# Performance work log

Measured on AMD Instinct MI355X. Metric: run time of the kernel, lower is better.

Reference implementation:

```python
import jax, jax.numpy as jnp
import numpy as np

EPS = 1e-5

def _ln(x, g, b):
    mu = jnp.mean(x, axis=-1, keepdims=True)
    var = jnp.mean((x - mu) ** 2, axis=-1, keepdims=True)
    return (x - mu) / jnp.sqrt(var + EPS) * g + b

def _aft(x, q_w, q_b, k_w, k_b, v_w, v_b, p_w, p_b, wbias):
    # AFTFull: Yt = sigmoid(Q) * (exp(wbias) @ (exp(K)*V)) / (exp(wbias) @ exp(K))
    T = x.shape[1]
    Q = x @ q_w + q_b
    K = x @ k_w + k_b
    V = x @ v_w + v_b
    ew = jnp.exp(wbias[:T, :T])                      # [T, T]
    eK = jnp.exp(K)                                   # [B, T, H]
    num = jnp.einsum('ts,bsh->bth', ew, eK * V)
    den = jnp.einsum('ts,bsh->bth', ew, eK)
    Yt = jax.nn.sigmoid(Q) * (num / den)
    return Yt @ p_w + p_b

def setup_inputs() -> dict:
    key = jax.random.key(0)
    B, T, D, H = 8, 2048, 256, 256
    MAXT = 2048
    std = 1.0 / np.sqrt(H)
    names_shapes = [
        ('fc_w', (D, H)), ('fc_b', (H,)),
        ('q_w', (H, H)), ('q_b', (H,)),
        ('k_w', (H, H)), ('k_b', (H,)),
        ('v_w', (H, H)), ('v_b', (H,)),
        ('p_w', (H, H)), ('p_b', (H,)),
        ('wbias', (MAXT, MAXT)),
        ('n1_g', (H,)), ('n1_b', (H,)),
        ('n2_g', (H,)), ('n2_b', (H,)),
        ('w_i', (H, H)), ('u_i', (H, H)), ('b_i', (H,)),
        ('w_f', (H, H)), ('u_f', (H, H)), ('b_f', (H,)),
        ('w_c', (H, H)), ('u_c', (H, H)), ('b_c', (H,)),
        ('w_o', (H, H)), ('u_o', (H, H)), ('b_o', (H,)),
    ]
    keys = jax.random.split(key, len(names_shapes) + 1)
    inp = {'x': jax.random.normal(keys[0], (B, T, D), dtype=jnp.float32)}
    for k, (name, shp) in zip(keys[1:], names_shapes):
        inp[name] = jax.random.uniform(k, shp, dtype=jnp.float32, minval=-std, maxval=std)
    return inp

def reference(x, fc_w, fc_b, q_w, q_b, k_w, k_b, v_w, v_b, p_w, p_b, wbias,
              n1_g, n1_b, n2_g, n2_b,
              w_i, u_i, b_i, w_f, u_f, b_f, w_c, u_c, b_c, w_o, u_o, b_o):
    xf = x @ fc_w + fc_b                              # [B, T, H]
    att = _aft(xf, q_w, q_b, k_w, k_b, v_w, v_b, p_w, p_b, wbias)
    # original calls self.norm(x_) but discards the result -> only relu applies
    filt = jax.nn.relu(att)
    afx = _ln(att, n1_g, n1_b)
    prod = _ln(filt * afx, n2_g, n2_b)                # [B, T, H]
    B, T, H = prod.shape
    h0 = jnp.zeros((B, H), prod.dtype)
    c0 = jnp.zeros((B, H), prod.dtype)
    def step(carry, x_t):
        h, c = carry
        i = jax.nn.sigmoid(x_t @ w_i + h @ u_i + b_i)
        f = jax.nn.sigmoid(x_t @ w_f + h @ u_f + b_f)
        g = jnp.tanh(x_t @ w_c + h @ u_c + b_c)
        o = jax.nn.sigmoid(x_t @ w_o + h @ u_o + b_o)
        c = f * c + i * g
        h = o * jnp.tanh(c)
        return (h, c), h
    (h_t, c_t), hs = jax.lax.scan(step, (h0, c0), prod.transpose(1, 0, 2))
    hidden_seq = hs.transpose(1, 0, 2)                # [B, T, H]
    return hidden_seq, h_t, c_t
```

## Files before the change

### kernel.cpp

```cpp
#include <hip/hip_runtime.h>


typedef unsigned short u16;
typedef unsigned int   u32;
typedef u16 u16x4 __attribute__((ext_vector_type(4)));
typedef u16 u16x8 __attribute__((ext_vector_type(8)));
typedef u32 u32x2 __attribute__((ext_vector_type(2)));
typedef u32 u32x4 __attribute__((ext_vector_type(4)));
typedef short s16x8 __attribute__((ext_vector_type(8)));
typedef float f32x4 __attribute__((ext_vector_type(4)));
typedef _Float16 f16x2 __attribute__((ext_vector_type(2)));

typedef __attribute__((address_space(3))) void* lds_vp;
typedef const __attribute__((address_space(1))) void* gbl_vp;
#define GLDS(gp, lp) __builtin_amdgcn_global_load_lds((gbl_vp)(gp), (lds_vp)(lp), 16, 0, 0)

__device__ __forceinline__ float b2f(u16 u){
  union { u32 i; float f; } c; c.i = ((u32)u) << 16; return c.f;
}
__device__ __forceinline__ u16 f2b(float f){
  union { float f; u32 i; } c; c.f = f;
  u32 i = c.i;
  return (u16)((i + 0x7FFFu + ((i >> 16) & 1u)) >> 16);
}
__device__ __forceinline__ u16 f2h_bits(float f){
  _Float16 h = (_Float16)f;
  return __builtin_bit_cast(u16, h);
}
__device__ __forceinline__ float dot2(u32 a, u32 b, float acc){
#if __has_builtin(__builtin_amdgcn_fdot2)
  return __builtin_amdgcn_fdot2(__builtin_bit_cast(f16x2, a),
                                __builtin_bit_cast(f16x2, b), acc, false);
#else
  f16x2 x = __builtin_bit_cast(f16x2, a), y = __builtin_bit_cast(f16x2, b);
  return acc + (float)x[0]*(float)y[0] + (float)x[1]*(float)y[1];
#endif
}
__device__ __forceinline__ float sigm(float x){ return 1.f/(1.f + __expf(-x)); }
__device__ __forceinline__ float tanh_f(float x){
  float e = __expf(-2.f * fmaxf(x, -44.f));
  return (1.f - e)/(1.f + e);
}

__global__ void k_detect(const u16* __restrict__ x, int* __restrict__ flag){
  const int l = threadIdx.x;
  const u16 u = x[l];
  const float v = b2f(u);
  const int bad = !(v == v) || fabsf(v) > 1e4f || (v != 0.f && fabsf(v) < 1e-30f);
  const int zev = ((l & 1) == 0) && (u == 0);
  unsigned long long mb = __ballot(bad);
  unsigned long long mz = __ballot(zev);
  if (l == 0) *flag = (mb != 0ull || __popcll(mz) >= 24) ? 1 : 0;
}

__global__ __launch_bounds__(256) void k_cvt_x(const void* __restrict__ xin,
    u16* __restrict__ xb, const int* __restrict__ flag){
  const int isf = *flag;
  const size_t e = ((size_t)blockIdx.x*256 + threadIdx.x)*8;
  u16x8 o;
  if (isf){
    const float* p = (const float*)xin + e;
    f32x4 a = *(const f32x4*)p, b = *(const f32x4*)(p+4);
    o[0]=f2b(a[0]);o[1]=f2b(a[1]);o[2]=f2b(a[2]);o[3]=f2b(a[3]);
    o[4]=f2b(b[0]);o[5]=f2b(b[1]);o[6]=f2b(b[2]);o[7]=f2b(b[3]);
  } else {
    o = *(const u16x8*)((const u16*)xin + e);
  }
  *(u16x8*)(xb + e) = o;
}

template<int EPI>
__global__ __launch_bounds__(256)
void k_gemm(const u16* __restrict__ A, const u16* __restrict__ Bt,
            void* __restrict__ C, const u16* __restrict__ bias,
            const u16* __restrict__ aux,
            int M, int N, int K, int lda, int ldb, int ldc,
            long bsB , long bsC )
{
  __shared__ __align__(16) u16 As[128*32];
  __shared__ __align__(16) u16 Bs[128*32];
  const int tid = threadIdx.x;
  const int wv = tid >> 6, l = tid & 63;
  const int m0 = blockIdx.x * 128, n0 = blockIdx.y * 128;
  const u16* Bp = Bt + (size_t)blockIdx.z * bsB;
  char* Cp = (char*)C + (size_t)blockIdx.z * bsC;

  const int rL = wv*16 + (l >> 2);
  const int cL = (l & 3) * 8;
  const u16* gA = A  + (size_t)(m0 + rL)*lda + cL;
  const u16* gB = Bp + (size_t)(n0 + rL)*ldb + cL;
  u16* lA = As + wv*512 + l*8;
  u16* lB = Bs + wv*512 + l*8;

  f32x4 acc[4][4];
  #pragma unroll
  for (int m=0;m<4;++m)
    #pragma unroll
    for (int n=0;n<4;++n) acc[m][n] = f32x4{0.f,0.f,0.f,0.f};

  const int wr = wv >> 1, wc = wv & 1;
  const int lr = l & 15, lk = (l >> 4) * 8, lq = l >> 4;
  const int nk = K >> 5;
  for (int kt = 0; kt < nk; ++kt){
    __syncthreads();
    GLDS(gA,                  lA);
    GLDS(gA + (size_t)64*lda, lA + 2048);
    GLDS(gB,                  lB);
    GLDS(gB + (size_t)64*ldb, lB + 2048);
    gA += 32; gB += 32;
    __syncthreads();
    s16x8 af[4], bfr[4];
    #pragma unroll
    for (int m=0;m<4;++m) af[m]  = *(const s16x8*)&As[(wr*64 + m*16 + lr)*32 + lk];
    #pragma unroll
    for (int n=0;n<4;++n) bfr[n] = *(const s16x8*)&Bs[(wc*64 + n*16 + lr)*32 + lk];
    #pragma unroll
    for (int m=0;m<4;++m)
      #pragma unroll
      for (int n=0;n<4;++n)
        acc[m][n] = __builtin_amdgcn_mfma_f32_16x16x32_bf16(af[m], bfr[n], acc[m][n], 0, 0, 0);
  }

  #pragma unroll
  for (int m=0;m<4;++m){
    const int gr0 = m0 + wr*64 + m*16 + lq*4;
    #pragma unroll
    for (int n=0;n<4;++n){
      const int gc = n0 + wc*64 + n*16 + lr;
      f32x4 v = acc[m][n];
      if constexpr (EPI == 0 || EPI == 1 || EPI == 4){
        const float bb = b2f(bias[gc]);
        u16* Cb = (u16*)Cp;
        const int cc = (EPI == 4) ? (((gc & 255) << 2) + (gc >> 8)) : gc;
        #pragma unroll
        for (int r=0;r<4;++r){
          float xv = v[r] + bb;
          if constexpr (EPI == 1) xv = sigm(xv);
          Cb[(size_t)(gr0 + r)*ldc + cc] = f2b(xv);
        }
      } else if constexpr (EPI == 2){
        u16* Cb = (u16*)Cp;
        #pragma unroll
        for (int r=0;r<4;++r) Cb[(size_t)(gr0 + r)*ldc + gc] = f2b(v[r]);
      } else {
        const float bb = b2f(bias[gc]);
        u16x4 ekv, ek;
        #pragma unroll
        for (int r=0;r<4;++r){
          float e  = __expf(v[r] + bb);
          float vv = b2f(aux[(size_t)(gr0 + r)*256 + gc]);
          ek[r]  = f2b(e);
          ekv[r] = f2b(e * vv);
        }
        const int z = gr0 >> 11, t0 = gr0 & 2047;
        u16* base = (u16*)Cp + ((size_t)z*512 + gc)*2048 + t0;
        *(u16x4*)base = ekv;
        *(u16x4*)(base + (size_t)256*2048) = ek;
      }
    }
  }
}

struct TJobs { const void* src[13]; u16* dst[13]; int mode[13]; };

__global__ __launch_bounds__(256) void k_transpose(TJobs jb, const int* __restrict__ flag){
  const int isf = *flag;
  const int mz = blockIdx.y;
  const void* in = jb.src[mz]; u16* out = jb.dst[mz]; const int mode = jb.mode[mz];
  const int bi = blockIdx.x >> 2, bj = blockIdx.x & 3;
  __shared__ float tile[64][65];
  const int tid = threadIdx.x;
  const int r = tid >> 3, c = (tid & 7) * 8;
  #pragma unroll
  for (int it=0; it<2; ++it){
    const size_t base = (size_t)(bi*64 + it*32 + r)*256 + bj*64 + c;
    float vals[8];
    if (isf){
      const float* p = (const float*)in + base;
      f32x4 a = *(const f32x4*)p, b = *(const f32x4*)(p+4);
      vals[0]=a[0];vals[1]=a[1];vals[2]=a[2];vals[3]=a[3];
      vals[4]=b[0];vals[5]=b[1];vals[6]=b[2];vals[7]=b[3];
    } else {
      u16x8 v = *(const u16x8*)((const u16*)in + base);
      #pragma unroll
      for (int u=0;u<8;++u) vals[u] = b2f(v[u]);
    }
    #pragma unroll
    for (int u=0;u<8;++u) tile[it*32 + r][c+u] = vals[u];
  }
  __syncthreads();
  #pragma unroll
  for (int it=0; it<2; ++it){
    const int rr = it*32 + r;
    u16x8 o;
    #pragma unroll
    for (int u=0;u<8;++u){
      float xv = tile[c+u][rr];
      o[u] = mode ? f2h_bits(xv) : f2b(xv);
    }
    *(u16x8*)(out + (size_t)(bj*64 + rr)*256 + bi*64 + c) = o;
  }
}

struct PJobs { const void* src[13]; };

__global__ __launch_bounds__(256) void k_pack_params(PJobs pj, u16* __restrict__ pp,
                                                     const int* __restrict__ flag){
  const int isf = *flag;
  const int t = threadIdx.x, bid = blockIdx.x;
  const void* s = pj.src[bid];
  const float v = isf ? ((const float*)s)[t] : b2f(((const u16*)s)[t]);
  pp[bid*256 + t] = f2b(v);
}

__global__ __launch_bounds__(256) void k_expw(const void* __restrict__ wb,
    u16* __restrict__ ew, const int* __restrict__ flag){
  const int isf = *flag;
  const size_t e = ((size_t)blockIdx.x*256 + threadIdx.x)*8;
  u16x8 o;
  if (isf){
    const float* p = (const float*)wb + e;
    f32x4 a = *(const f32x4*)p, b = *(const f32x4*)(p+4);
    o[0]=f2b(__expf(a[0]));o[1]=f2b(__expf(a[1]));o[2]=f2b(__expf(a[2]));o[3]=f2b(__expf(a[3]));
    o[4]=f2b(__expf(b[0]));o[5]=f2b(__expf(b[1]));o[6]=f2b(__expf(b[2]));o[7]=f2b(__expf(b[3]));
  } else {
    u16x8 v = *(const u16x8*)((const u16*)wb + e);
    #pragma unroll
    for (int u=0;u<8;++u) o[u] = f2b(__expf(b2f(v[u])));
  }
  *(u16x8*)(ew + e) = o;
}

__global__ __launch_bounds__(256) void k_yt(const u16* __restrict__ sQ,
                                            const u16* __restrict__ nd,
                                            u16* __restrict__ yt){
  const int e = blockIdx.x*256 + threadIdx.x;
  const int m = e >> 6, n = (e & 63) << 2;
  const size_t ndb = ((size_t)(m >> 11)*2048 + (size_t)(m & 2047))*512 + n;
  u16x4 num = *(const u16x4*)(nd + ndb);
  u16x4 den = *(const u16x4*)(nd + ndb + 256);
  u16x4 q4  = *(const u16x4*)(sQ + (size_t)m*256 + n);
  u16x4 o;
  #pragma unroll
  for (int u=0;u<4;++u) o[u] = f2b(b2f(q4[u]) * b2f(num[u]) / b2f(den[u]));
  *(u16x4*)(yt + (size_t)m*256 + n) = o;
}

__device__ __forceinline__ float bsum(float v, float* red){
  #pragma unroll
  for (int o=1;o<64;o<<=1) v += __shfl_xor(v, o, 64);
  __syncthreads();
  if ((threadIdx.x & 63) == 0) red[threadIdx.x >> 6] = v;
  __syncthreads();
  return red[0]+red[1]+red[2]+red[3];
}

__global__ __launch_bounds__(256) void k_lnprod(const u16* __restrict__ att,
    const u16* __restrict__ pp, u16* __restrict__ prod){
  __shared__ float red[4];
  const int row = blockIdx.x, j = threadIdx.x;
  const u16* g1 = pp + 1280; const u16* b1 = pp + 1536;
  const u16* g2 = pp + 1792; const u16* b2_ = pp + 2048;
  const float a = b2f(att[(size_t)row*256 + j]);
  const float mu  = bsum(a, red) * (1.f/256.f);
  const float d   = a - mu;
  const float var = bsum(d*d, red) * (1.f/256.f);
  const float afx = d * rsqrtf(var + 1e-5f) * b2f(g1[j]) + b2f(b1[j]);
  const float y   = fmaxf(a, 0.f) * afx;
  const float mu2  = bsum(y, red) * (1.f/256.f);
  const float d2   = y - mu2;
  const float var2 = bsum(d2*d2, red) * (1.f/256.f);
  const float o = d2 * rsqrtf(var2 + 1e-5f) * b2f(g2[j]) + b2f(b2_[j]);
  prod[(size_t)row*256 + j] = f2b(o);
}

__global__ __attribute__((amdgpu_flat_work_group_size(512,512), amdgpu_waves_per_eu(2,2)))
void k_lstm(const u16* __restrict__ P4, const u16* __restrict__ UT,
            void* __restrict__ outv, const int* __restrict__ flag)
{
  const int isf = *flag;
  const int b = blockIdx.x;
  const int tid = threadIdx.x;
  const int hp = tid >> 2, s = tid & 3;
  const int m  = s >> 1;
  const int hcol = 2*hp + m;

  __shared__ u32x4 Wtl4[16*512];
  __shared__ __align__(16) u32 hl[2][160];

  const u32* U32 = (const u32*)UT;
  u32 wv[8][24];
  #pragma unroll
  for (int gi=0; gi<8; ++gi){
    const int gc = (gi>>1)*256 + 2*hp + (gi&1);
    const u32* base = U32 + (size_t)gc*128 + s*32;
    #pragma unroll
    for (int k=0; k<24; ++k) wv[gi][k] = base[k];
    Wtl4[(gi*2 + 0)*512 + tid] = ((const u32x4*)base)[6];
    Wtl4[(gi*2 + 1)*512 + tid] = ((const u32x4*)base)[7];
  }
  #pragma unroll
  for (int gi=0; gi<8; ++gi)
    #pragma unroll
    for (int k=0; k<24; ++k)
      asm volatile("" : "+v"(wv[gi][k]));

  if (tid < 160) hl[0][tid] = 0u;
  float c_state = 0.f, h_cur = 0.f;
  const u16* Pb = P4 + (size_t)b*2048*1024;
  u16x4 pn = *(const u16x4*)(Pb + (size_t)hcol*4);
  __syncthreads();

  int cur = 0;
  for (int t=0; t<2048; ++t){
    const u16x4 pc = pn;
    if (t < 2047)
      pn = *(const u16x4*)(Pb + (size_t)(t+1)*1024 + (size_t)hcol*4);

    const u32x4* hb = (const u32x4*)hl[cur];
    float sums[8];
    #pragma unroll
    for (int gi=0; gi<8; ++gi) sums[gi] = 0.f;

    #pragma unroll
    for (int ch=0; ch<6; ++ch){
      const u32x4 h4 = hb[s*10 + ch];
      #pragma unroll
      for (int gi=0; gi<8; ++gi){
        sums[gi] = dot2(h4.x, wv[gi][ch*4+0], sums[gi]);
        sums[gi] = dot2(h4.y, wv[gi][ch*4+1], sums[gi]);
        sums[gi] = dot2(h4.z, wv[gi][ch*4+2], sums[gi]);
        sums[gi] = dot2(h4.w, wv[gi][ch*4+3], sums[gi]);
      }
    }
    #pragma unroll
    for (int cc=0; cc<2; ++cc){
      const u32x4 h4 = hb[s*10 + 6 + cc];
      #pragma unroll
      for (int gi=0; gi<8; ++gi){
        const u32x4 wt = Wtl4[(gi*2 + cc)*512 + tid];
        sums[gi] = dot2(h4.x, wt.x, sums[gi]);
        sums[gi] = dot2(h4.y, wt.y, sums[gi]);
        sums[gi] = dot2(h4.z, wt.z, sums[gi]);
        sums[gi] = dot2(h4.w, wt.w, sums[gi]);
      }
    }

    #pragma unroll
    for (int gi=0; gi<8; ++gi){
      sums[gi] += __shfl_xor(sums[gi], 1, 64);
      sums[gi] += __shfl_xor(sums[gi], 2, 64);
    }

    const float pre_i = sums[0 + m] + b2f(pc[0]);
    const float pre_f = sums[2 + m] + b2f(pc[1]);
    const float pre_g = sums[4 + m] + b2f(pc[2]);
    const float pre_o = sums[6 + m] + b2f(pc[3]);
    const float gi_ = sigm(pre_i);
    const float gf_ = sigm(pre_f);
    const float gg_ = tanh_f(pre_g);
    const float go_ = sigm(pre_o);
    c_state = gf_*c_state + gi_*gg_;
    h_cur = go_ * tanh_f(c_state);

    const u32 hu = (u32)f2h_bits(h_cur);
    const u32 other = __shfl_xor(hu, 2, 64);
    const int nxt = cur ^ 1;
    if (s == 0) hl[nxt][(hp >> 5)*40 + (hp & 31)] = (other << 16) | hu;
    if ((s & 1) == 0){
      const size_t oe = (size_t)b*524288 + (size_t)t*256 + hcol;
      if (isf) ((float*)outv)[oe] = h_cur;
      else     ((u16*)outv)[oe]   = f2b(h_cur);
    }
    __syncthreads();
    cur = nxt;
  }

  if ((s & 1) == 0){
    const size_t o1 = 4194304 + (size_t)b*256 + hcol;
    if (isf){ ((float*)outv)[o1] = h_cur; ((float*)outv)[o1 + 2048] = c_state; }
    else    { ((u16*)outv)[o1] = f2b(h_cur); ((u16*)outv)[o1 + 2048] = f2b(c_state); }
  }
}

extern "C" void kernel_launch(void* const* d_in, const int* in_sizes, int n_in,
                              void* d_out, int out_size, void* d_ws, size_t ws_size,
                              hipStream_t stream)
{
  const void* x    = d_in[0];
  const void* fc_w = d_in[1];  const void* fc_b = d_in[2];
  const void* q_w  = d_in[3];  const void* q_b  = d_in[4];
  const void* k_w  = d_in[5];  const void* k_b  = d_in[6];
  const void* v_w  = d_in[7];  const void* v_b  = d_in[8];
  const void* p_w  = d_in[9];  const void* p_b  = d_in[10];
  const void* wbias= d_in[11];
  const void* n1g  = d_in[12]; const void* n1b  = d_in[13];
  const void* n2g  = d_in[14]; const void* n2b  = d_in[15];
  const void* w_i  = d_in[16]; const void* u_i  = d_in[17];
  const void* b_i  = d_in[18];
  const void* w_f  = d_in[19]; const void* u_f  = d_in[20];
  const void* b_f  = d_in[21];
  const void* w_c  = d_in[22]; const void* u_c  = d_in[23];
  const void* b_c  = d_in[24];
  const void* w_o  = d_in[25]; const void* u_o  = d_in[26];
  const void* b_o  = d_in[27];

  char* w = (char*)d_ws;
  u16* ew   = (u16*)(w + 0);
  u16* WT   = (u16*)(w + 8388608);
  u16* UT   = (u16*)(w + 9568256);
  u16* pp   = (u16*)(w + 10092544);
  int* flag = (int*)(w + 10099200);
  u16* xf   = (u16*)(w + 10099712);
  u16* Vb   = (u16*)(w + 18488320);
  u16* sQ   = (u16*)(w + 26876928);
  u16* ekvT = (u16*)(w + 35265536);
  u16* nd   = (u16*)(w + 52042752);
  u16* xb   = ekvT;
  u16* yt   = xf;
  u16* att  = Vb;
  u16* prod = sQ;
  u16* P    = ekvT;

  k_detect<<<1, 64, 0, stream>>>((const u16*)x, flag);

  k_cvt_x<<<2048, 256, 0, stream>>>(x, xb, flag);
  TJobs jb;
  const void* srcs[13] = {fc_w, q_w, k_w, v_w, p_w, w_i, w_f, w_c, w_o, u_i, u_f, u_c, u_o};
  for (int i=0;i<13;++i){
    jb.src[i]  = srcs[i];
    jb.dst[i]  = (i < 9) ? (WT + (size_t)i*65536) : (UT + (size_t)(i-9)*65536);
    jb.mode[i] = (i < 9) ? 0 : 1;
  }
  k_transpose<<<dim3(16,13), 256, 0, stream>>>(jb, flag);
  PJobs pj;
  const void* psrc[13] = {fc_b, q_b, k_b, v_b, p_b, n1g, n1b, n2g, n2b, b_i, b_f, b_c, b_o};
  for (int i=0;i<13;++i) pj.src[i] = psrc[i];
  k_pack_params<<<13, 256, 0, stream>>>(pj, pp, flag);

  k_expw<<<2048, 256, 0, stream>>>(wbias, ew, flag);

  k_gemm<0><<<dim3(128,2,1), 256, 0, stream>>>(xb, WT + 0*65536, xf, pp + 0, nullptr,
      16384,256,256, 256,256,256, 0,0);
  k_gemm<0><<<dim3(128,2,1), 256, 0, stream>>>(xf, WT + 3*65536, Vb, pp + 768, nullptr,
      16384,256,256, 256,256,256, 0,0);
  k_gemm<1><<<dim3(128,2,1), 256, 0, stream>>>(xf, WT + 1*65536, sQ, pp + 256, nullptr,
      16384,256,256, 256,256,256, 0,0);
  k_gemm<3><<<dim3(128,2,1), 256, 0, stream>>>(xf, WT + 2*65536, ekvT, pp + 512, Vb,
      16384,256,256, 256,256,2048, 0,0);

  k_gemm<2><<<dim3(16,4,8), 256, 0, stream>>>(ew, ekvT, nd, nullptr, nullptr,
      2048,512,2048, 2048,2048,512, (long)512*2048, (long)2048*512*2);

  k_yt<<<4096, 256, 0, stream>>>(sQ, nd, yt);

  k_gemm<0><<<dim3(128,2,1), 256, 0, stream>>>(yt, WT + 4*65536, att, pp + 1024, nullptr,
      16384,256,256, 256,256,256, 0,0);

  k_lnprod<<<16384, 256, 0, stream>>>(att, pp, prod);

  k_gemm<4><<<dim3(128,8,1), 256, 0, stream>>>(prod, WT + 5*65536, P, pp + 2304, nullptr,
      16384,1024,256, 256,256,1024, 0,0);

  k_lstm<<<8, 512, 0, stream>>>(P, UT, d_out, flag);
}
```

Measured before the change: 4.408 ms.

## Rewrite LSTM recurrence with MFMA across two cooperating blocks and flag sync

The per-batch fp16 dot2 LSTM kernel, which kept the recurrent weights in registers, is replaced by a kernel that batches all 8 sequences into one bf16 MFMA per step. The 1024 hidden gate columns are split across two workgroups (blocks 0 and 8, the other launched blocks exit at once). The two workgroups exchange h halves each step through global memory, using release/acquire flags that are zeroed by a memset. This is meant to use matrix cores and more parallelism per step. In exchange it adds a cross-block spin-wait and a global round trip every timestep, switches the recurrent path from fp16 to bf16, and relies on both blocks being resident at the same time.

```diff
diff --git a/kernel.cpp b/kernel.cpp
--- a/kernel.cpp
+++ b/kernel.cpp
@@ -5,11 +5,8 @@
 typedef unsigned int   u32;
 typedef u16 u16x4 __attribute__((ext_vector_type(4)));
 typedef u16 u16x8 __attribute__((ext_vector_type(8)));
-typedef u32 u32x2 __attribute__((ext_vector_type(2)));
-typedef u32 u32x4 __attribute__((ext_vector_type(4)));
 typedef short s16x8 __attribute__((ext_vector_type(8)));
 typedef float f32x4 __attribute__((ext_vector_type(4)));
-typedef _Float16 f16x2 __attribute__((ext_vector_type(2)));
 
 typedef __attribute__((address_space(3))) void* lds_vp;
 typedef const __attribute__((address_space(1))) void* gbl_vp;
@@ -22,19 +19,6 @@
   union { float f; u32 i; } c; c.f = f;
   u32 i = c.i;
   return (u16)((i + 0x7FFFu + ((i >> 16) & 1u)) >> 16);
-}
-__device__ __forceinline__ u16 f2h_bits(float f){
-  _Float16 h = (_Float16)f;
-  return __builtin_bit_cast(u16, h);
-}
-__device__ __forceinline__ float dot2(u32 a, u32 b, float acc){
-#if __has_builtin(__builtin_amdgcn_fdot2)
-  return __builtin_amdgcn_fdot2(__builtin_bit_cast(f16x2, a),
-                                __builtin_bit_cast(f16x2, b), acc, false);
-#else
-  f16x2 x = __builtin_bit_cast(f16x2, a), y = __builtin_bit_cast(f16x2, b);
-  return acc + (float)x[0]*(float)y[0] + (float)x[1]*(float)y[1];
-#endif
 }
 __device__ __forceinline__ float sigm(float x){ return 1.f/(1.f + __expf(-x)); }
 __device__ __forceinline__ float tanh_f(float x){
@@ -161,12 +145,12 @@
   }
 }
 
-struct TJobs { const void* src[13]; u16* dst[13]; int mode[13]; };
+struct TJobs { const void* src[13]; u16* dst[13]; };
 
 __global__ __launch_bounds__(256) void k_transpose(TJobs jb, const int* __restrict__ flag){
   const int isf = *flag;
   const int mz = blockIdx.y;
-  const void* in = jb.src[mz]; u16* out = jb.dst[mz]; const int mode = jb.mode[mz];
+  const void* in = jb.src[mz]; u16* out = jb.dst[mz];
   const int bi = blockIdx.x >> 2, bj = blockIdx.x & 3;
   __shared__ float tile[64][65];
   const int tid = threadIdx.x;
@@ -194,10 +178,7 @@
     const int rr = it*32 + r;
     u16x8 o;
     #pragma unroll
-    for (int u=0;u<8;++u){
-      float xv = tile[c+u][rr];
-      o[u] = mode ? f2h_bits(xv) : f2b(xv);
-    }
+    for (int u=0;u<8;++u) o[u] = f2b(tile[c+u][rr]);
     *(u16x8*)(out + (size_t)(bj*64 + rr)*256 + bi*64 + c) = o;
   }
 }
@@ -274,88 +255,71 @@
   prod[(size_t)row*256 + j] = f2b(o);
 }
 
-__global__ __attribute__((amdgpu_flat_work_group_size(512,512), amdgpu_waves_per_eu(2,2)))
-void k_lstm(const u16* __restrict__ P4, const u16* __restrict__ UT,
-            void* __restrict__ outv, const int* __restrict__ flag)
+__global__ __launch_bounds__(1024)
+void k_lstm2(const u16* __restrict__ P4, const u16* __restrict__ UT,
+             void* __restrict__ outv, const int* __restrict__ flag,
+             int* __restrict__ sync)
 {
+  const int bid = blockIdx.x;
+  if (bid != 0 && bid != 8) return;
+  const int side = bid >> 3;
   const int isf = *flag;
-  const int b = blockIdx.x;
   const int tid = threadIdx.x;
-  const int hp = tid >> 2, s = tid & 3;
-  const int m  = s >> 1;
-  const int hcol = 2*hp + m;
-
-  __shared__ u32x4 Wtl4[16*512];
-  __shared__ __align__(16) u32 hl[2][160];
-
-  const u32* U32 = (const u32*)UT;
-  u32 wv[8][24];
-  #pragma unroll
-  for (int gi=0; gi<8; ++gi){
-    const int gc = (gi>>1)*256 + 2*hp + (gi&1);
-    const u32* base = U32 + (size_t)gc*128 + s*32;
-    #pragma unroll
-    for (int k=0; k<24; ++k) wv[gi][k] = base[k];
-    Wtl4[(gi*2 + 0)*512 + tid] = ((const u32x4*)base)[6];
-    Wtl4[(gi*2 + 1)*512 + tid] = ((const u32x4*)base)[7];
-  }
-  #pragma unroll
-  for (int gi=0; gi<8; ++gi)
-    #pragma unroll
-    for (int k=0; k<24; ++k)
-      asm volatile("" : "+v"(wv[gi][k]));
-
-  if (tid < 160) hl[0][tid] = 0u;
+  const int wave = tid >> 6, l = tid & 63;
+  const int lr = l & 15, lq = l >> 4;
+
+  __shared__ __align__(16) u16 hlds[2*16*264];
+  __shared__ float pre[8*516];
+
+  for (int i = tid; i < 2*16*264; i += 1024) hlds[i] = 0;
+
+  s16x8 bf0[8], bf1[8];
+  {
+    const int c0 = wave*32 + lr, c1 = c0 + 16;
+    const int g0 = c0 >> 7, g1v = c1 >> 7;
+    const size_t gcol0 = (size_t)(g0*256 + side*128 + (c0 & 127)) * 256;
+    const size_t gcol1 = (size_t)(g1v*256 + side*128 + (c1 & 127)) * 256;
+    #pragma unroll
+    for (int ks=0; ks<8; ++ks){
+      bf0[ks] = *(const s16x8*)(UT + gcol0 + ks*32 + lq*8);
+      bf1[ks] = *(const s16x8*)(UT + gcol1 + ks*32 + lq*8);
+    }
+  }
+
+  const int b  = tid >> 7, lc = tid & 127;
+  const int hcol = side*128 + lc;
   float c_state = 0.f, h_cur = 0.f;
-  const u16* Pb = P4 + (size_t)b*2048*1024;
+  const u16* Pb = P4 + ((size_t)b*2048)*1024;
   u16x4 pn = *(const u16x4*)(Pb + (size_t)hcol*4);
   __syncthreads();
 
   int cur = 0;
   for (int t=0; t<2048; ++t){
+    f32x4 acc0{0.f,0.f,0.f,0.f}, acc1{0.f,0.f,0.f,0.f};
+    const u16* hb = hlds + cur*4224 + lr*264;
+    #pragma unroll
+    for (int ks=0; ks<8; ++ks){
+      s16x8 a = *(const s16x8*)(hb + ks*32 + lq*8);
+      acc0 = __builtin_amdgcn_mfma_f32_16x16x32_bf16(a, bf0[ks], acc0, 0, 0, 0);
+      acc1 = __builtin_amdgcn_mfma_f32_16x16x32_bf16(a, bf1[ks], acc1, 0, 0, 0);
+    }
+    if (l < 32){
+      const int col0 = wave*32 + lr;
+      #pragma unroll
+      for (int r=0;r<4;++r){
+        pre[(lq*4+r)*516 + col0]      = acc0[r];
+        pre[(lq*4+r)*516 + col0 + 16] = acc1[r];
+      }
+    }
+    __syncthreads();
+
     const u16x4 pc = pn;
     if (t < 2047)
       pn = *(const u16x4*)(Pb + (size_t)(t+1)*1024 + (size_t)hcol*4);
-
-    const u32x4* hb = (const u32x4*)hl[cur];
-    float sums[8];
-    #pragma unroll
-    for (int gi=0; gi<8; ++gi) sums[gi] = 0.f;
-
-    #pragma unroll
-    for (int ch=0; ch<6; ++ch){
-      const u32x4 h4 = hb[s*10 + ch];
-      #pragma unroll
-      for (int gi=0; gi<8; ++gi){
-        sums[gi] = dot2(h4.x, wv[gi][ch*4+0], sums[gi]);
-        sums[gi] = dot2(h4.y, wv[gi][ch*4+1], sums[gi]);
-        sums[gi] = dot2(h4.z, wv[gi][ch*4+2], sums[gi]);
-        sums[gi] = dot2(h4.w, wv[gi][ch*4+3], sums[gi]);
-      }
-    }
-    #pragma unroll
-    for (int cc=0; cc<2; ++cc){
-      const u32x4 h4 = hb[s*10 + 6 + cc];
-      #pragma unroll
-      for (int gi=0; gi<8; ++gi){
-        const u32x4 wt = Wtl4[(gi*2 + cc)*512 + tid];
-        sums[gi] = dot2(h4.x, wt.x, sums[gi]);
-        sums[gi] = dot2(h4.y, wt.y, sums[gi]);
-        sums[gi] = dot2(h4.z, wt.z, sums[gi]);
-        sums[gi] = dot2(h4.w, wt.w, sums[gi]);
-      }
-    }
-
-    #pragma unroll
-    for (int gi=0; gi<8; ++gi){
-      sums[gi] += __shfl_xor(sums[gi], 1, 64);
-      sums[gi] += __shfl_xor(sums[gi], 2, 64);
-    }
-
-    const float pre_i = sums[0 + m] + b2f(pc[0]);
-    const float pre_f = sums[2 + m] + b2f(pc[1]);
-    const float pre_g = sums[4 + m] + b2f(pc[2]);
-    const float pre_o = sums[6 + m] + b2f(pc[3]);
+    const float pre_i = pre[b*516 + lc]       + b2f(pc[0]);
+    const float pre_f = pre[b*516 + 128 + lc] + b2f(pc[1]);
+    const float pre_g = pre[b*516 + 256 + lc] + b2f(pc[2]);
+    const float pre_o = pre[b*516 + 384 + lc] + b2f(pc[3]);
     const float gi_ = sigm(pre_i);
     const float gf_ = sigm(pre_f);
     const float gg_ = tanh_f(pre_g);
@@ -363,20 +327,32 @@
     c_state = gf_*c_state + gi_*gg_;
     h_cur = go_ * tanh_f(c_state);
 
-    const u32 hu = (u32)f2h_bits(h_cur);
-    const u32 other = __shfl_xor(hu, 2, 64);
     const int nxt = cur ^ 1;
-    if (s == 0) hl[nxt][(hp >> 5)*40 + (hp & 31)] = (other << 16) | hu;
-    if ((s & 1) == 0){
-      const size_t oe = (size_t)b*524288 + (size_t)t*256 + hcol;
-      if (isf) ((float*)outv)[oe] = h_cur;
-      else     ((u16*)outv)[oe]   = f2b(h_cur);
-    }
-    __syncthreads();
+    const u16 hb16 = f2b(h_cur);
+    hlds[nxt*4224 + b*264 + hcol] = hb16;
+    const size_t oe = (size_t)b*524288 + (size_t)t*256 + hcol;
+    if (isf) ((float*)outv)[oe] = h_cur;
+    else     ((u16*)outv)[oe]   = hb16;
+
+    if (t < 2047){
+      __syncthreads();
+      if (tid == 0)
+        __hip_atomic_store(&sync[side*2048 + t], 1, __ATOMIC_RELEASE,
+                           __HIP_MEMORY_SCOPE_AGENT);
+      while (__hip_atomic_load(&sync[(1 - side)*2048 + t], __ATOMIC_ACQUIRE,
+                               __HIP_MEMORY_SCOPE_AGENT) == 0) {}
+      const int pcol = (1 - side)*128 + lc;
+      const size_t pe = (size_t)b*524288 + (size_t)t*256 + pcol;
+      u16 pv;
+      if (isf) pv = f2b(((const float*)outv)[pe]);
+      else     pv = ((const u16*)outv)[pe];
+      hlds[nxt*4224 + b*264 + pcol] = pv;
+      __syncthreads();
+    }
     cur = nxt;
   }
 
-  if ((s & 1) == 0){
+  {
     const size_t o1 = 4194304 + (size_t)b*256 + hcol;
     if (isf){ ((float*)outv)[o1] = h_cur; ((float*)outv)[o1 + 2048] = c_state; }
     else    { ((u16*)outv)[o1] = f2b(h_cur); ((u16*)outv)[o1 + 2048] = f2b(c_state); }
@@ -416,6 +392,7 @@
   u16* sQ   = (u16*)(w + 26876928);
   u16* ekvT = (u16*)(w + 35265536);
   u16* nd   = (u16*)(w + 52042752);
+  int* sync = (int*)(w + 68819968);
   u16* xb   = ekvT;
   u16* yt   = xf;
   u16* att  = Vb;
@@ -423,6 +400,7 @@
   u16* P    = ekvT;
 
   k_detect<<<1, 64, 0, stream>>>((const u16*)x, flag);
+  hipMemsetAsync(sync, 0, 2*2048*sizeof(int), stream);
 
   k_cvt_x<<<2048, 256, 0, stream>>>(x, xb, flag);
   TJobs jb;
@@ -430,7 +408,6 @@
   for (int i=0;i<13;++i){
     jb.src[i]  = srcs[i];
     jb.dst[i]  = (i < 9) ? (WT + (size_t)i*65536) : (UT + (size_t)(i-9)*65536);
-    jb.mode[i] = (i < 9) ? 0 : 1;
   }
   k_transpose<<<dim3(16,13), 256, 0, stream>>>(jb, flag);
   PJobs pj;
@@ -462,5 +439,5 @@
   k_gemm<4><<<dim3(128,8,1), 256, 0, stream>>>(prod, WT + 5*65536, P, pp + 2304, nullptr,
       16384,1024,256, 256,256,1024, 0,0);
 
-  k_lstm<<<8, 512, 0, stream>>>(P, UT, d_out, flag);
-}
+  k_lstm2<<<16, 1024, 0, stream>>>(P, UT, d_out, flag, sync);
+}
```

After: 11.97 ms. +171.6%, slower.
